# Optimization experiments

Hardware: AMD Instinct MI355X
Metric: run time of the kernel (lower is better)

Reference implementation:

```python
import jax, jax.numpy as jnp
import numpy as np

B, S, P, E, H, FF = 4, 16, 256, 768, 12, 3072
HD = E // H
LN_EPS = 1e-5


def _layernorm(x, g, b):
    m = jnp.mean(x, axis=-1, keepdims=True)
    v = jnp.mean((x - m) ** 2, axis=-1, keepdims=True)
    return (x - m) * jax.lax.rsqrt(v + LN_EPS) * g + b


def _qkv(x, wqkv, bqkv):
    # wqkv: [3, E, E] (in, out layout), bqkv: [3, E]
    qkv = jnp.einsum('bspe,tef->tbspf', x, wqkv) + bqkv[:, None, None, None, :]
    q, k, v = qkv
    b, s, p, e = x.shape
    shp = (b, s, p, H, HD)
    return q.reshape(shp), k.reshape(shp), v.reshape(shp)


def spatial_attn(x, wqkv, bqkv, wo, bo, g, beta):
    q, k, v = _qkv(x, wqkv, bqkv)  # [b,s,p,n,d]
    scale = 1.0 / np.sqrt(HD).astype(np.float32)
    scores = jnp.einsum('bsind,bsjnd->bsnij', q, k) * scale  # [b,s,n,p,p]
    attn = jax.nn.softmax(scores, axis=-1)
    out = jnp.einsum('bsnij,bsjnd->bsind', attn, v)  # [b,s,p,n,d]
    out = out.reshape(x.shape)
    out = out @ wo + bo
    return _layernorm(x + out, g, beta)


def temporal_attn(x, wqkv, bqkv, wo, bo, g, beta):
    q, k, v = _qkv(x, wqkv, bqkv)  # [b,s,p,n,d]
    scale = 1.0 / np.sqrt(HD).astype(np.float32)
    scores = jnp.einsum('bipnd,bjpnd->bpnij', q, k) * scale  # [b,p,n,s,s]
    s = x.shape[1]
    causal = jnp.tril(jnp.ones((s, s), dtype=bool))
    scores = jnp.where(causal, scores, jnp.float32(-jnp.inf))
    attn = jax.nn.softmax(scores, axis=-1)
    out = jnp.einsum('bpnij,bjpnd->bipnd', attn, v)  # [b,s,p,n,d]
    out = out.reshape(x.shape)
    out = out @ wo + bo
    return _layernorm(x + out, g, beta)


def ffn(x, w1, b1, w2, b2, g, beta):
    h = jax.nn.relu(x @ w1 + b1)
    out = h @ w2 + b2
    return _layernorm(x + out, g, beta)


def setup_inputs() -> dict:
    key = jax.random.key(0)
    ks = jax.random.split(key, 16)
    w = lambda k, shp: (jax.random.normal(k, shp, dtype=jnp.float32) * 0.02)
    inp = {
        'x': jax.random.normal(ks[0], (B, S, P, E), dtype=jnp.float32),
        'sa_wqkv': w(ks[1], (3, E, E)), 'sa_bqkv': jnp.zeros((3, E), jnp.float32),
        'sa_wo': w(ks[2], (E, E)), 'sa_bo': jnp.zeros((E,), jnp.float32),
        'sa_g': jnp.ones((E,), jnp.float32), 'sa_b': jnp.zeros((E,), jnp.float32),
        'ta_wqkv': w(ks[3], (3, E, E)), 'ta_bqkv': jnp.zeros((3, E), jnp.float32),
        'ta_wo': w(ks[4], (E, E)), 'ta_bo': jnp.zeros((E,), jnp.float32),
        'ta_g': jnp.ones((E,), jnp.float32), 'ta_b': jnp.zeros((E,), jnp.float32),
        'f_w1': w(ks[5], (E, FF)), 'f_b1': jnp.zeros((FF,), jnp.float32),
        'f_w2': w(ks[6], (FF, E)), 'f_b2': jnp.zeros((E,), jnp.float32),
        'f_g': jnp.ones((E,), jnp.float32), 'f_b': jnp.zeros((E,), jnp.float32),
    }
    return inp


def reference(x, sa_wqkv, sa_bqkv, sa_wo, sa_bo, sa_g, sa_b,
              ta_wqkv, ta_bqkv, ta_wo, ta_bo, ta_g, ta_b,
              f_w1, f_b1, f_w2, f_b2, f_g, f_b):
    x = spatial_attn(x, sa_wqkv, sa_bqkv, sa_wo, sa_bo, sa_g, sa_b)
    x = temporal_attn(x, ta_wqkv, ta_bqkv, ta_wo, ta_bo, ta_g, ta_b)
    x = ffn(x, f_w1, f_b1, f_w2, f_b2, f_g, f_b)
    return x
```

## Files before the change

### kernel.cpp

```cpp
#include <hip/hip_runtime.h>
#include <hip/hip_bf16.h>
#include <math.h>

constexpr int Bc = 4, Sc = 16, Pc = 256, Ec = 768, Hc = 12, HDc = 64, FFc = 3072;
constexpr int Mrows = Bc * Sc * Pc;
constexpr size_t ME = (size_t)Mrows * Ec;

typedef __attribute__((ext_vector_type(4))) float f32x4;
typedef __attribute__((ext_vector_type(8))) short s16x8;
typedef __attribute__((ext_vector_type(4))) short s16x4;

__device__ __forceinline__ short f2bf(float f) {
  union { float f; unsigned u; } v; v.f = f;
  unsigned r = (v.u + 0x7FFFu + ((v.u >> 16) & 1u)) >> 16;
  return (short)r;
}
__device__ __forceinline__ float bf2f(short s) {
  union { unsigned u; float f; } v; v.u = ((unsigned)(unsigned short)s) << 16;
  return v.f;
}

__device__ __forceinline__ void async16(const void* g, void* l) {
  __builtin_amdgcn_global_load_lds(
      (const __attribute__((address_space(1))) unsigned int*)g,
      (__attribute__((address_space(3))) unsigned int*)l, 16, 0, 0);
}

__global__ __launch_bounds__(256)
void f2bf_kernel(const float* __restrict__ in, short* __restrict__ out, int n8)
{
  int i = blockIdx.x * 256 + threadIdx.x;
  if (i >= n8) return;
  const float4* p = reinterpret_cast<const float4*>(in + (size_t)i * 8);
  float4 a = p[0], b = p[1];
  s16x8 o = { f2bf(a.x), f2bf(a.y), f2bf(a.z), f2bf(a.w),
              f2bf(b.x), f2bf(b.y), f2bf(b.z), f2bf(b.w) };
  *reinterpret_cast<s16x8*>(out + (size_t)i * 8) = o;
}

__global__ __launch_bounds__(256)
void wtrans_kernel(const float* __restrict__ Wg, short* __restrict__ Wtg,
                   int K, int N)
{
  const int z = blockIdx.z;
  const float* W  = Wg  + (size_t)z * K * N;
  short*       Wt = Wtg + (size_t)z * N * K;
  const int n0 = blockIdx.x * 64, k0 = blockIdx.y * 64;
  const int t = threadIdx.x;
  const int n  = n0 + (t >> 2);
  const int kc = k0 + (t & 3) * 16;
  short buf[16];
#pragma unroll
  for (int i = 0; i < 16; ++i)
    buf[i] = f2bf(W[(size_t)(kc + i) * N + n]);
  *reinterpret_cast<s16x8*>(&Wt[(size_t)n * K + kc])     = *reinterpret_cast<s16x8*>(&buf[0]);
  *reinterpret_cast<s16x8*>(&Wt[(size_t)n * K + kc + 8]) = *reinterpret_cast<s16x8*>(&buf[8]);
}

#define LDFRAG(base, row, kc) \
  (*reinterpret_cast<const s16x8*>((base) + (row) * 128 + ((((kc) ^ ((row) & 7)) << 4))))

#define PH_READS(Aslot, Bslot, q, LDB) \
  do { \
    if (LDB) { \
      _Pragma("unroll") \
      for (int nj = 0; nj < 4; ++nj) { \
        bfr[nj][0] = LDFRAG((Bslot), wc * 64 + nj * 16 + l16, g); \
        bfr[nj][1] = LDFRAG((Bslot), wc * 64 + nj * 16 + l16, 4 + g); \
      } \
    } \
    _Pragma("unroll") \
    for (int mi = 0; mi < 2; ++mi) { \
      afr[mi][0] = LDFRAG((Aslot), wr * 128 + ((q) * 2 + mi) * 16 + l16, g); \
      afr[mi][1] = LDFRAG((Aslot), wr * 128 + ((q) * 2 + mi) * 16 + l16, 4 + g); \
    } \
  } while (0)

#define PH_SYNC_MMA(q) \
  do { \
    __builtin_amdgcn_sched_barrier(0); \
    __builtin_amdgcn_s_barrier(); \
    asm volatile("s_waitcnt lgkmcnt(0)" ::: "memory"); \
    __builtin_amdgcn_sched_barrier(0); \
    __builtin_amdgcn_s_setprio(1); \
    _Pragma("unroll") \
    for (int mi = 0; mi < 2; ++mi) \
      _Pragma("unroll") \
      for (int nj = 0; nj < 4; ++nj) { \
        acc[(q) * 2 + mi][nj] = __builtin_amdgcn_mfma_f32_16x16x32_bf16( \
            afr[mi][0], bfr[nj][0], acc[(q) * 2 + mi][nj], 0, 0, 0); \
        acc[(q) * 2 + mi][nj] = __builtin_amdgcn_mfma_f32_16x16x32_bf16( \
            afr[mi][1], bfr[nj][1], acc[(q) * 2 + mi][nj], 0, 0, 0); \
      } \
    __builtin_amdgcn_s_setprio(0); \
  } while (0)

#define PH_END \
  do { __builtin_amdgcn_s_barrier(); __builtin_amdgcn_sched_barrier(0); } while (0)

#define PH_END_VM \
  do { \
    asm volatile("s_waitcnt vmcnt(4)" ::: "memory"); \
    __builtin_amdgcn_sched_barrier(0); \
    __builtin_amdgcn_s_barrier(); \
    __builtin_amdgcn_sched_barrier(0); \
  } while (0)

template<int OUT>
__global__ __launch_bounds__(512, 2)
void gemm256_kernel(const short* __restrict__ A, const short* __restrict__ Wt,
                    const float* __restrict__ biasg, const void* __restrict__ resv,
                    void* __restrict__ Cg, short* __restrict__ vt,
                    int M, int N, int K)
{
  __shared__ char smem[131072];
  const int z = blockIdx.z;
  const short* __restrict__ Wz = Wt + (size_t)z * (size_t)N * K;
  const float* __restrict__ bz = biasg + (size_t)z * N;

  const int nwg = gridDim.x;
  const int swz = ((int)blockIdx.x & 7) * (nwg >> 3) + ((int)blockIdx.x >> 3);
  const int NT = N >> 8;
  const int bm = (swz / NT) << 8;
  const int bn = (swz % NT) << 8;

  const int tid  = threadIdx.x;
  const int lane = tid & 63;
  const int wid  = tid >> 6;
  const int wr   = wid >> 2;
  const int wc   = wid & 3;
  const int l16  = lane & 15;
  const int g    = lane >> 4;

  char* const As0 = smem;
  char* const Bs0 = smem + 32768;
  char* const As1 = smem + 65536;
  char* const Bs1 = smem + 98304;

  const int srow = lane >> 3;
  const int scol = ((lane & 7) ^ srow) * 8;
  const int ldso = wid * 1024;

  auto stageG = [&](const short* __restrict__ G, int grow0, int k0, char* ldsHalf) {
    const size_t r0 = (size_t)(grow0 + wid * 8 + srow);
    async16(G + r0 * K + (k0 + scol), ldsHalf + ldso);
    async16(G + (r0 + 64) * K + (k0 + scol), ldsHalf + 8192 + ldso);
  };

  f32x4 acc[8][4];
  s16x8 bfr[4][2];
  s16x8 afr[2][2];
#pragma unroll
  for (int mi = 0; mi < 8; ++mi)
#pragma unroll
    for (int nj = 0; nj < 4; ++nj) acc[mi][nj] = f32x4{0.f, 0.f, 0.f, 0.f};

  const int ntile = K >> 6;
  const int nit   = ntile >> 1;

  stageG(A,  bm,        0,  As0);
  stageG(A,  bm + 128,  0,  As0 + 16384);
  stageG(Wz, bn,        0,  Bs0);
  stageG(Wz, bn + 128,  0,  Bs0 + 16384);
  stageG(Wz, bn,        64, Bs1);
  stageG(Wz, bn + 128,  64, Bs1 + 16384);
  asm volatile("s_waitcnt vmcnt(4)" ::: "memory");
  __builtin_amdgcn_sched_barrier(0);
  __builtin_amdgcn_s_barrier();

  for (int j = 0; j < nit; ++j) {
    const int t1k = (2 * j + 1) << 6;
    const int t2k = (2 * j + 2) << 6;
    const int t3k = (2 * j + 3) << 6;
    const bool s2 = (2 * j + 2) < ntile;
    const bool s3 = (2 * j + 3) < ntile;

    PH_READS(As0, Bs0, 0, true);
    stageG(A, bm, t1k, As1);
    PH_SYNC_MMA(0);
    PH_END;

    PH_READS(As0, Bs0, 1, false);
    stageG(A, bm + 128, t1k, As1 + 16384);
    PH_SYNC_MMA(1);
    PH_END;

    PH_READS(As0, Bs0, 2, false);
    if (s2) stageG(Wz, bn, t2k, Bs0);
    PH_SYNC_MMA(2);
    PH_END;

    PH_READS(As0, Bs0, 3, false);
    if (s2) stageG(Wz, bn + 128, t2k, Bs0 + 16384);
    PH_SYNC_MMA(3);
    PH_END_VM;

    PH_READS(As1, Bs1, 0, true);
    if (s2) stageG(A, bm, t2k, As0);
    PH_SYNC_MMA(0);
    PH_END;

    PH_READS(As1, Bs1, 1, false);
    if (s2) stageG(A, bm + 128, t2k, As0 + 16384);
    PH_SYNC_MMA(1);
    PH_END;

    PH_READS(As1, Bs1, 2, false);
    if (s3) stageG(Wz, bn, t3k, Bs1);
    PH_SYNC_MMA(2);
    PH_END;

    PH_READS(As1, Bs1, 3, false);
    if (s3) stageG(Wz, bn + 128, t3k, Bs1 + 16384);
    PH_SYNC_MMA(3);
    PH_END_VM;
  }

  const float* resf = (const float*)resv;
  const short* resb = (const short*)resv;
  short* Cb = (short*)Cg + (size_t)z * (size_t)M * N;
  float* Cf = (float*)Cg + (size_t)z * (size_t)M * N;

#pragma unroll
  for (int mi = 0; mi < 8; ++mi) {
    const int row0 = bm + wr * 128 + mi * 16 + g * 4;
#pragma unroll
    for (int nj = 0; nj < 4; ++nj) {
      const int col = bn + wc * 64 + nj * 16 + l16;
      if (OUT == 4 && z == 2) {
        const int bs2 = row0 >> 8, p0 = row0 & 255;
        const int h2 = col >> 6,  d2 = col & 63;
        const float bias = bz[col];
        s16x4 v = { f2bf(acc[mi][nj][0] + bias), f2bf(acc[mi][nj][1] + bias),
                    f2bf(acc[mi][nj][2] + bias), f2bf(acc[mi][nj][3] + bias) };
        *reinterpret_cast<s16x4*>(
            &vt[(((size_t)bs2 * 12 + h2) * 64 + d2) * 256 + p0]) = v;
      } else {
        const float bias = bz[col];
#pragma unroll
        for (int r = 0; r < 4; ++r) {
          float v = acc[mi][nj][r] + bias;
          size_t idx = (size_t)(row0 + r) * N + col;
          if (OUT == 2) v += resf[idx];
          if (OUT == 3) v += bf2f(resb[idx]);
          if (OUT == 1) v = fmaxf(v, 0.f);
          if (OUT == 2 || OUT == 3) Cf[idx] = v;
          else                      Cb[idx] = f2bf(v);
        }
      }
    }
  }
}

__global__ __launch_bounds__(256, 3)
void spatial_attn_kernel(const short* __restrict__ Qg, const short* __restrict__ Kg,
                         const short* __restrict__ Vt, short* __restrict__ Og)
{
  const int bs = blockIdx.x;
  const int h  = blockIdx.y;

  __shared__ short Pl[4 * 32 * 64];

  const int tid  = threadIdx.x;
  const int lane = tid & 63;
  const int wid  = tid >> 6;
  const int l16  = lane & 15;
  const int g    = lane >> 4;
  const int q0   = blockIdx.z * 128 + wid * 32;
  char* Pw = (char*)Pl + wid * 4096;

  const size_t rowbase = (size_t)(bs * 256) * 768 + h * 64;
  const size_t vbase   = ((size_t)bs * 12 + h) * 64 * 256;

  s16x8 qa[2][2];
#pragma unroll
  for (int m = 0; m < 2; ++m)
#pragma unroll
    for (int ks = 0; ks < 2; ++ks)
      qa[m][ks] = *reinterpret_cast<const s16x8*>(
          &Qg[rowbase + (size_t)(q0 + m * 16 + l16) * 768 + ks * 32 + g * 8]);

  float mrun[2][4], lrun[2][4];
  f32x4 oac[2][4];
#pragma unroll
  for (int m = 0; m < 2; ++m)
#pragma unroll
    for (int r = 0; r < 4; ++r) { mrun[m][r] = -INFINITY; lrun[m][r] = 0.f; }
#pragma unroll
  for (int m = 0; m < 2; ++m)
#pragma unroll
    for (int n = 0; n < 4; ++n) oac[m][n] = f32x4{0.f, 0.f, 0.f, 0.f};

#pragma unroll
  for (int t = 0; t < 4; ++t) {
    const int key0 = t * 64;
    f32x4 sc[2][4];
#pragma unroll
    for (int m = 0; m < 2; ++m)
#pragma unroll
      for (int n = 0; n < 4; ++n) sc[m][n] = f32x4{0.f, 0.f, 0.f, 0.f};
#pragma unroll
    for (int ks = 0; ks < 2; ++ks) {
      s16x8 kf[4];
#pragma unroll
      for (int n = 0; n < 4; ++n) {
        const int key = key0 + n * 16 + l16;
        kf[n] = *reinterpret_cast<const s16x8*>(
            &Kg[rowbase + (size_t)key * 768 + ks * 32 + g * 8]);
      }
#pragma unroll
      for (int m = 0; m < 2; ++m)
#pragma unroll
        for (int n = 0; n < 4; ++n)
          sc[m][n] = __builtin_amdgcn_mfma_f32_16x16x32_bf16(qa[m][ks], kf[n], sc[m][n], 0, 0, 0);
    }
#pragma unroll
    for (int m = 0; m < 2; ++m)
#pragma unroll
      for (int n = 0; n < 4; ++n)
#pragma unroll
        for (int r = 0; r < 4; ++r) sc[m][n][r] *= 0.125f;

#pragma unroll
    for (int m = 0; m < 2; ++m) {
#pragma unroll
      for (int r = 0; r < 4; ++r) {
        float mx = fmaxf(fmaxf(sc[m][0][r], sc[m][1][r]), fmaxf(sc[m][2][r], sc[m][3][r]));
#pragma unroll
        for (int mk = 1; mk < 16; mk <<= 1) mx = fmaxf(mx, __shfl_xor(mx, mk, 64));
        const float mnew = fmaxf(mrun[m][r], mx);
        const float corr = __expf(mrun[m][r] - mnew);
        mrun[m][r] = mnew;
        float rs = 0.f;
#pragma unroll
        for (int n = 0; n < 4; ++n) {
          float p = __expf(sc[m][n][r] - mnew);
          sc[m][n][r] = p;
          rs += p;
        }
#pragma unroll
        for (int mk = 1; mk < 16; mk <<= 1) rs += __shfl_xor(rs, mk, 64);
        lrun[m][r] = lrun[m][r] * corr + rs;
#pragma unroll
        for (int nd = 0; nd < 4; ++nd) oac[m][nd][r] *= corr;
      }
    }
#pragma unroll
    for (int m = 0; m < 2; ++m)
#pragma unroll
      for (int n = 0; n < 4; ++n)
#pragma unroll
        for (int r = 0; r < 4; ++r) {
          const int q = m * 16 + g * 4 + r;
          const int key = n * 16 + l16;
          const int byte = q * 128 + (((key >> 3) ^ (q & 7)) * 16) + (key & 7) * 2;
          *reinterpret_cast<short*>(Pw + byte) = f2bf(sc[m][n][r]);
        }
#pragma unroll
    for (int ks = 0; ks < 2; ++ks) {
      s16x8 pa[2], vf[4];
#pragma unroll
      for (int m = 0; m < 2; ++m) {
        const int q = m * 16 + l16;
        const int s = ks * 4 + g;
        pa[m] = *reinterpret_cast<const s16x8*>(Pw + q * 128 + ((s ^ (q & 7)) * 16));
      }
#pragma unroll
      for (int nd = 0; nd < 4; ++nd) {
        const int d = nd * 16 + l16;
        const int key = key0 + ks * 32 + g * 8;
        vf[nd] = *reinterpret_cast<const s16x8*>(&Vt[vbase + (size_t)d * 256 + key]);
      }
#pragma unroll
      for (int m = 0; m < 2; ++m)
#pragma unroll
        for (int nd = 0; nd < 4; ++nd)
          oac[m][nd] = __builtin_amdgcn_mfma_f32_16x16x32_bf16(pa[m], vf[nd], oac[m][nd], 0, 0, 0);
    }
  }

#pragma unroll
  for (int m = 0; m < 2; ++m)
#pragma unroll
    for (int r = 0; r < 4; ++r) {
      const float inv = 1.f / lrun[m][r];
#pragma unroll
      for (int nd = 0; nd < 4; ++nd) oac[m][nd][r] *= inv;
    }
#pragma unroll
  for (int m = 0; m < 2; ++m)
#pragma unroll
    for (int nd = 0; nd < 4; ++nd)
#pragma unroll
      for (int r = 0; r < 4; ++r) {
        const int q = m * 16 + g * 4 + r;
        const int d = nd * 16 + l16;
        const int byte = q * 128 + (((d >> 3) ^ (q & 7)) * 16) + (d & 7) * 2;
        *reinterpret_cast<short*>(Pw + byte) = f2bf(oac[m][nd][r]);
      }
#pragma unroll
  for (int it = 0; it < 4; ++it) {
    const int slot = it * 64 + lane;
    const int q = slot >> 3, sl = slot & 7;
    const int d0 = (sl ^ (q & 7)) * 8;
    s16x8 v = *reinterpret_cast<const s16x8*>(Pw + slot * 16);
    *reinterpret_cast<s16x8*>(
        &Og[rowbase + (size_t)(q0 + q) * 768 + d0]) = v;
  }
}

__global__ __launch_bounds__(192)
void temporal_attn_kernel(const short* __restrict__ Qg, const short* __restrict__ Kg,
                          const short* __restrict__ Vg, short* __restrict__ Og)
{
  const int bp = blockIdx.x;
  const int b = bp >> 8, p = bp & 255;
  const int tid = threadIdx.x;
  const int h = tid >> 4, i = tid & 15;

  const float scale = 0.125f;
  auto rowoff = [&](int s) {
    return ((size_t)(b * Sc + s) * Pc + p) * Ec + (size_t)h * HDc;
  };

  float q[HDc];
  {
    const short* qp = &Qg[rowoff(i)];
#pragma unroll
    for (int c = 0; c < 8; ++c) {
      s16x8 v = *reinterpret_cast<const s16x8*>(qp + c * 8);
#pragma unroll
      for (int e = 0; e < 8; ++e) q[c * 8 + e] = bf2f(v[e]) * scale;
    }
  }
  float m = -INFINITY, l = 0.f;
  float o[HDc];
#pragma unroll
  for (int d = 0; d < HDc; ++d) o[d] = 0.f;

  for (int j = 0; j <= i; ++j) {
    const short* kp = &Kg[rowoff(j)];
    float s = 0.f;
#pragma unroll
    for (int c = 0; c < 8; ++c) {
      s16x8 kv = *reinterpret_cast<const s16x8*>(kp + c * 8);
#pragma unroll
      for (int e = 0; e < 8; ++e) s += q[c * 8 + e] * bf2f(kv[e]);
    }
    float mn   = fmaxf(m, s);
    float corr = __expf(m - mn);
    float pw   = __expf(s - mn);
    l = l * corr + pw;
    const short* vp = &Vg[rowoff(j)];
#pragma unroll
    for (int c = 0; c < 8; ++c) {
      s16x8 vv = *reinterpret_cast<const s16x8*>(vp + c * 8);
#pragma unroll
      for (int e = 0; e < 8; ++e)
        o[c * 8 + e] = fmaf(pw, bf2f(vv[e]), o[c * 8 + e] * corr);
    }
    m = mn;
  }
  const float inv = 1.f / l;
  short* op = &Og[rowoff(i)];
#pragma unroll
  for (int c = 0; c < 8; ++c) {
    s16x8 v;
#pragma unroll
    for (int e = 0; e < 8; ++e) v[e] = f2bf(o[c * 8 + e] * inv);
    *reinterpret_cast<s16x8*>(op + c * 8) = v;
  }
}

template<bool OUTBF>
__global__ __launch_bounds__(256)
void layernorm_kernel(const float* __restrict__ U, const float* __restrict__ g,
                      const float* __restrict__ be, void* __restrict__ outv)
{
  const int tid  = threadIdx.x;
  const int lane = tid & 63, w = tid >> 6;
  const size_t row = (size_t)blockIdx.x * 4 + w;
  const float* u = U + row * Ec;

  float x[12];
#pragma unroll
  for (int c = 0; c < 3; ++c) {
    float4 v = *reinterpret_cast<const float4*>(&u[c * 256 + lane * 4]);
    x[c*4+0] = v.x; x[c*4+1] = v.y; x[c*4+2] = v.z; x[c*4+3] = v.w;
  }
  float s = 0.f;
#pragma unroll
  for (int k = 0; k < 12; ++k) s += x[k];
#pragma unroll
  for (int off = 32; off > 0; off >>= 1) s += __shfl_xor(s, off, 64);
  const float mean = s * (1.f / 768.f);

  float vs = 0.f;
#pragma unroll
  for (int k = 0; k < 12; ++k) { float d = x[k] - mean; vs += d * d; }
#pragma unroll
  for (int off = 32; off > 0; off >>= 1) vs += __shfl_xor(vs, off, 64);
  const float rs = rsqrtf(vs * (1.f / 768.f) + 1e-5f);

#pragma unroll
  for (int c = 0; c < 3; ++c) {
    int idx = c * 256 + lane * 4;
    float4 gv = *reinterpret_cast<const float4*>(&g[idx]);
    float4 bv = *reinterpret_cast<const float4*>(&be[idx]);
    float r0 = (x[c*4+0] - mean) * rs * gv.x + bv.x;
    float r1 = (x[c*4+1] - mean) * rs * gv.y + bv.y;
    float r2 = (x[c*4+2] - mean) * rs * gv.z + bv.z;
    float r3 = (x[c*4+3] - mean) * rs * gv.w + bv.w;
    if (OUTBF) {
      short* op = (short*)outv + row * Ec + idx;
      s16x4 v = { f2bf(r0), f2bf(r1), f2bf(r2), f2bf(r3) };
      *reinterpret_cast<s16x4*>(op) = v;
    } else {
      float* op = (float*)outv + row * Ec + idx;
      *reinterpret_cast<float4*>(op) = make_float4(r0, r1, r2, r3);
    }
  }
}

extern "C" void kernel_launch(void* const* d_in, const int* in_sizes, int n_in,
                              void* d_out, int out_size, void* d_ws, size_t ws_size,
                              hipStream_t stream)
{
  const float* x       = (const float*)d_in[0];
  const float* sa_wqkv = (const float*)d_in[1];
  const float* sa_bqkv = (const float*)d_in[2];
  const float* sa_wo   = (const float*)d_in[3];
  const float* sa_bo   = (const float*)d_in[4];
  const float* sa_g    = (const float*)d_in[5];
  const float* sa_b    = (const float*)d_in[6];
  const float* ta_wqkv = (const float*)d_in[7];
  const float* ta_bqkv = (const float*)d_in[8];
  const float* ta_wo   = (const float*)d_in[9];
  const float* ta_bo   = (const float*)d_in[10];
  const float* ta_g    = (const float*)d_in[11];
  const float* ta_b    = (const float*)d_in[12];
  const float* f_w1    = (const float*)d_in[13];
  const float* f_b1    = (const float*)d_in[14];
  const float* f_w2    = (const float*)d_in[15];
  const float* f_b2    = (const float*)d_in[16];
  const float* f_g     = (const float*)d_in[17];
  const float* f_b     = (const float*)d_in[18];

  float* out = (float*)d_out;

  constexpr size_t EE = (size_t)Ec * Ec;
  constexpr size_t WTOT = 3*EE + EE + 3*EE + EE + 2*(size_t)Ec*FFc;
  const size_t need = 14 * ME + 2 * WTOT;
  if (ws_size < need) return;

  short* Xb  = (short*)d_ws;
  short* Qb  = Xb + ME;
  short* Kb  = Qb + ME;
  short* Vtb = Qb + 2 * ME;
  short* Hb  = Qb;
  float* U   = (float*)(Xb + 5 * ME);
  short* Wtb = (short*)(U + ME);

  short* wt_sa_qkv = Wtb;
  short* wt_sa_wo  = wt_sa_qkv + 3 * EE;
  short* wt_ta_qkv = wt_sa_wo  + EE;
  short* wt_ta_wo  = wt_ta_qkv + 3 * EE;
  short* wt_f_w1   = wt_ta_wo  + EE;
  short* wt_f_w2   = wt_f_w1   + (size_t)Ec * FFc;

  wtrans_kernel<<<dim3(12, 12, 3), 256, 0, stream>>>(sa_wqkv, wt_sa_qkv, Ec, Ec);
  wtrans_kernel<<<dim3(12, 12, 1), 256, 0, stream>>>(sa_wo,   wt_sa_wo,  Ec, Ec);
  wtrans_kernel<<<dim3(12, 12, 3), 256, 0, stream>>>(ta_wqkv, wt_ta_qkv, Ec, Ec);
  wtrans_kernel<<<dim3(12, 12, 1), 256, 0, stream>>>(ta_wo,   wt_ta_wo,  Ec, Ec);
  wtrans_kernel<<<dim3(48, 12, 1), 256, 0, stream>>>(f_w1,    wt_f_w1,   Ec, FFc);
  wtrans_kernel<<<dim3(12, 48, 1), 256, 0, stream>>>(f_w2,    wt_f_w2,   FFc, Ec);
  f2bf_kernel<<<(int)(ME / 8 / 256), 256, 0, stream>>>(x, Xb, (int)(ME / 8));

  const int MT = Mrows / 256;
  const dim3 gQKV(MT * (Ec / 256), 1, 3);
  const dim3 gSQ (MT * (Ec / 256), 1, 1);
  const dim3 gFF1(MT * (FFc / 256), 1, 1);

  gemm256_kernel<4><<<gQKV, 512, 0, stream>>>(Xb, wt_sa_qkv, sa_bqkv, nullptr, Qb, Vtb, Mrows, Ec, Ec);
  spatial_attn_kernel<<<dim3(Bc * Sc, Hc, 2), 256, 0, stream>>>(Qb, Kb, Vtb, Qb);
  gemm256_kernel<2><<<gSQ, 512, 0, stream>>>(Qb, wt_sa_wo, sa_bo, x, U, nullptr, Mrows, Ec, Ec);
  layernorm_kernel<true><<<Mrows / 4, 256, 0, stream>>>(U, sa_g, sa_b, Xb);

  gemm256_kernel<0><<<gQKV, 512, 0, stream>>>(Xb, wt_ta_qkv, ta_bqkv, nullptr, Qb, nullptr, Mrows, Ec, Ec);
  temporal_attn_kernel<<<Bc * Pc, 192, 0, stream>>>(Qb, Kb, Vtb, Qb);
  gemm256_kernel<3><<<gSQ, 512, 0, stream>>>(Qb, wt_ta_wo, ta_bo, Xb, U, nullptr, Mrows, Ec, Ec);
  layernorm_kernel<true><<<Mrows / 4, 256, 0, stream>>>(U, ta_g, ta_b, Xb);

  gemm256_kernel<1><<<gFF1, 512, 0, stream>>>(Xb, wt_f_w1, f_b1, nullptr, Hb, nullptr, Mrows, FFc, Ec);
  gemm256_kernel<3><<<gSQ, 512, 0, stream>>>(Hb, wt_f_w2, f_b2, Xb, U, nullptr, Mrows, Ec, FFc);
  layernorm_kernel<false><<<Mrows / 4, 256, 0, stream>>>(U, f_g, f_b, out);
}
```

Baseline: 643.2 us.

## Use 128-row GEMM tiles for N=768 projections and stage temporal K/V in LDS

The GEMM kernel gains a BMT template parameter so the output projections and the FFN2 GEMM (N=768) run with 128x256 tiles. This doubles the grid for those launches, aiming to fill more CUs and reduce tail imbalance, at the cost of less reuse of the weight tile. The temporal attention kernel now cooperatively loads all 16 timesteps of K and V for one (b,p) into shared memory with a head-interleaved layout. The causal loop then reads LDS instead of repeatedly hitting global memory from each thread. Threads are remapped to head-fastest order (h = tid%12) for this.

Result: faster. 613.5 us (-4.6%).

```diff
diff --git a/kernel.cpp b/kernel.cpp
--- a/kernel.cpp
+++ b/kernel.cpp
@@ -70,9 +70,10 @@
       } \
     } \
     _Pragma("unroll") \
-    for (int mi = 0; mi < 2; ++mi) { \
-      afr[mi][0] = LDFRAG((Aslot), wr * 128 + ((q) * 2 + mi) * 16 + l16, g); \
-      afr[mi][1] = LDFRAG((Aslot), wr * 128 + ((q) * 2 + mi) * 16 + l16, 4 + g); \
+    for (int mi = 0; mi < BMT; ++mi) { \
+      const int arow = wr * (BMT * 64) + ((q) * BMT + mi) * 16 + l16; \
+      afr[mi][0] = LDFRAG((Aslot), arow, g); \
+      afr[mi][1] = LDFRAG((Aslot), arow, 4 + g); \
     } \
   } while (0)
 
@@ -84,13 +85,13 @@
     __builtin_amdgcn_sched_barrier(0); \
     __builtin_amdgcn_s_setprio(1); \
     _Pragma("unroll") \
-    for (int mi = 0; mi < 2; ++mi) \
+    for (int mi = 0; mi < BMT; ++mi) \
       _Pragma("unroll") \
       for (int nj = 0; nj < 4; ++nj) { \
-        acc[(q) * 2 + mi][nj] = __builtin_amdgcn_mfma_f32_16x16x32_bf16( \
-            afr[mi][0], bfr[nj][0], acc[(q) * 2 + mi][nj], 0, 0, 0); \
-        acc[(q) * 2 + mi][nj] = __builtin_amdgcn_mfma_f32_16x16x32_bf16( \
-            afr[mi][1], bfr[nj][1], acc[(q) * 2 + mi][nj], 0, 0, 0); \
+        acc[(q) * BMT + mi][nj] = __builtin_amdgcn_mfma_f32_16x16x32_bf16( \
+            afr[mi][0], bfr[nj][0], acc[(q) * BMT + mi][nj], 0, 0, 0); \
+        acc[(q) * BMT + mi][nj] = __builtin_amdgcn_mfma_f32_16x16x32_bf16( \
+            afr[mi][1], bfr[nj][1], acc[(q) * BMT + mi][nj], 0, 0, 0); \
       } \
     __builtin_amdgcn_s_setprio(0); \
   } while (0)
@@ -106,14 +107,15 @@
     __builtin_amdgcn_sched_barrier(0); \
   } while (0)
 
-template<int OUT>
+template<int OUT, int BMT>
 __global__ __launch_bounds__(512, 2)
 void gemm256_kernel(const short* __restrict__ A, const short* __restrict__ Wt,
                     const float* __restrict__ biasg, const void* __restrict__ resv,
                     void* __restrict__ Cg, short* __restrict__ vt,
                     int M, int N, int K)
 {
-  __shared__ char smem[131072];
+  constexpr int ASZ = BMT * 16384;
+  __shared__ char smem[2 * (ASZ + 32768)];
   const int z = blockIdx.z;
   const short* __restrict__ Wz = Wt + (size_t)z * (size_t)N * K;
   const float* __restrict__ bz = biasg + (size_t)z * N;
@@ -121,7 +123,7 @@
   const int nwg = gridDim.x;
   const int swz = ((int)blockIdx.x & 7) * (nwg >> 3) + ((int)blockIdx.x >> 3);
   const int NT = N >> 8;
-  const int bm = (swz / NT) << 8;
+  const int bm = (swz / NT) * (BMT * 128);
   const int bn = (swz % NT) << 8;
 
   const int tid  = threadIdx.x;
@@ -133,9 +135,9 @@
   const int g    = lane >> 4;
 
   char* const As0 = smem;
-  char* const Bs0 = smem + 32768;
-  char* const As1 = smem + 65536;
-  char* const Bs1 = smem + 98304;
+  char* const Bs0 = smem + ASZ;
+  char* const As1 = smem + ASZ + 32768;
+  char* const Bs1 = smem + 2 * ASZ + 32768;
 
   const int srow = lane >> 3;
   const int scol = ((lane & 7) ^ srow) * 8;
@@ -147,23 +149,23 @@
     async16(G + (r0 + 64) * K + (k0 + scol), ldsHalf + 8192 + ldso);
   };
 
-  f32x4 acc[8][4];
+  f32x4 acc[BMT * 4][4];
   s16x8 bfr[4][2];
-  s16x8 afr[2][2];
-#pragma unroll
-  for (int mi = 0; mi < 8; ++mi)
+  s16x8 afr[BMT][2];
+#pragma unroll
+  for (int mi = 0; mi < BMT * 4; ++mi)
 #pragma unroll
     for (int nj = 0; nj < 4; ++nj) acc[mi][nj] = f32x4{0.f, 0.f, 0.f, 0.f};
 
   const int ntile = K >> 6;
   const int nit   = ntile >> 1;
 
-  stageG(A,  bm,        0,  As0);
-  stageG(A,  bm + 128,  0,  As0 + 16384);
-  stageG(Wz, bn,        0,  Bs0);
-  stageG(Wz, bn + 128,  0,  Bs0 + 16384);
-  stageG(Wz, bn,        64, Bs1);
-  stageG(Wz, bn + 128,  64, Bs1 + 16384);
+  stageG(A, bm, 0, As0);
+  if (BMT == 2) stageG(A, bm + 128, 0, As0 + 16384);
+  stageG(Wz, bn,       0,  Bs0);
+  stageG(Wz, bn + 128, 0,  Bs0 + 16384);
+  stageG(Wz, bn,       64, Bs1);
+  stageG(Wz, bn + 128, 64, Bs1 + 16384);
   asm volatile("s_waitcnt vmcnt(4)" ::: "memory");
   __builtin_amdgcn_sched_barrier(0);
   __builtin_amdgcn_s_barrier();
@@ -181,7 +183,7 @@
     PH_END;
 
     PH_READS(As0, Bs0, 1, false);
-    stageG(A, bm + 128, t1k, As1 + 16384);
+    if (BMT == 2) stageG(A, bm + 128, t1k, As1 + 16384);
     PH_SYNC_MMA(1);
     PH_END;
 
@@ -201,7 +203,7 @@
     PH_END;
 
     PH_READS(As1, Bs1, 1, false);
-    if (s2) stageG(A, bm + 128, t2k, As0 + 16384);
+    if (BMT == 2) { if (s2) stageG(A, bm + 128, t2k, As0 + 16384); }
     PH_SYNC_MMA(1);
     PH_END;
 
@@ -222,8 +224,8 @@
   float* Cf = (float*)Cg + (size_t)z * (size_t)M * N;
 
 #pragma unroll
-  for (int mi = 0; mi < 8; ++mi) {
-    const int row0 = bm + wr * 128 + mi * 16 + g * 4;
+  for (int mi = 0; mi < BMT * 4; ++mi) {
+    const int row0 = bm + wr * (BMT * 64) + mi * 16 + g * 4;
 #pragma unroll
     for (int nj = 0; nj < 4; ++nj) {
       const int col = bn + wc * 64 + nj * 16 + l16;
@@ -415,35 +417,54 @@
 {
   const int bp = blockIdx.x;
   const int b = bp >> 8, p = bp & 255;
+
+  __shared__ short Ks[16 * 768];
+  __shared__ short Vs[16 * 768];
+
   const int tid = threadIdx.x;
-  const int h = tid >> 4, i = tid & 15;
-
+  const size_t gbase = ((size_t)(b * 16) * 256 + p) * 768;
+  constexpr int SROW = 256 * 768;
+
+  {
+    const int half = tid / 96;
+    const int cc   = tid - half * 96;
+    const int c    = cc & 7, hs = cc >> 3;
+    const int ldso = (c * 12 + hs) * 8;
+#pragma unroll
+    for (int it = 0; it < 8; ++it) {
+      const int s = it * 2 + half;
+      const size_t ga = gbase + (size_t)s * SROW + cc * 8;
+      *reinterpret_cast<s16x8*>(&Ks[s * 768 + ldso]) =
+          *reinterpret_cast<const s16x8*>(&Kg[ga]);
+      *reinterpret_cast<s16x8*>(&Vs[s * 768 + ldso]) =
+          *reinterpret_cast<const s16x8*>(&Vg[ga]);
+    }
+  }
+  __syncthreads();
+
+  const int h = tid % 12, i = tid / 12;
   const float scale = 0.125f;
-  auto rowoff = [&](int s) {
-    return ((size_t)(b * Sc + s) * Pc + p) * Ec + (size_t)h * HDc;
-  };
+  const size_t qoff = gbase + (size_t)i * SROW + h * 64;
 
   float q[HDc];
-  {
-    const short* qp = &Qg[rowoff(i)];
-#pragma unroll
-    for (int c = 0; c < 8; ++c) {
-      s16x8 v = *reinterpret_cast<const s16x8*>(qp + c * 8);
-#pragma unroll
-      for (int e = 0; e < 8; ++e) q[c * 8 + e] = bf2f(v[e]) * scale;
-    }
-  }
+#pragma unroll
+  for (int c = 0; c < 8; ++c) {
+    s16x8 v = *reinterpret_cast<const s16x8*>(&Qg[qoff + c * 8]);
+#pragma unroll
+    for (int e = 0; e < 8; ++e) q[c * 8 + e] = bf2f(v[e]) * scale;
+  }
+
   float m = -INFINITY, l = 0.f;
   float o[HDc];
 #pragma unroll
   for (int d = 0; d < HDc; ++d) o[d] = 0.f;
 
   for (int j = 0; j <= i; ++j) {
-    const short* kp = &Kg[rowoff(j)];
+    const short* kr = &Ks[j * 768];
     float s = 0.f;
 #pragma unroll
     for (int c = 0; c < 8; ++c) {
-      s16x8 kv = *reinterpret_cast<const s16x8*>(kp + c * 8);
+      s16x8 kv = *reinterpret_cast<const s16x8*>(kr + (c * 12 + h) * 8);
 #pragma unroll
       for (int e = 0; e < 8; ++e) s += q[c * 8 + e] * bf2f(kv[e]);
     }
@@ -451,10 +472,10 @@
     float corr = __expf(m - mn);
     float pw   = __expf(s - mn);
     l = l * corr + pw;
-    const short* vp = &Vg[rowoff(j)];
+    const short* vr = &Vs[j * 768];
 #pragma unroll
     for (int c = 0; c < 8; ++c) {
-      s16x8 vv = *reinterpret_cast<const s16x8*>(vp + c * 8);
+      s16x8 vv = *reinterpret_cast<const s16x8*>(vr + (c * 12 + h) * 8);
 #pragma unroll
       for (int e = 0; e < 8; ++e)
         o[c * 8 + e] = fmaf(pw, bf2f(vv[e]), o[c * 8 + e] * corr);
@@ -462,7 +483,7 @@
     m = mn;
   }
   const float inv = 1.f / l;
-  short* op = &Og[rowoff(i)];
+  short* op = &Og[qoff];
 #pragma unroll
   for (int c = 0; c < 8; ++c) {
     s16x8 v;
@@ -576,22 +597,21 @@
   wtrans_kernel<<<dim3(12, 48, 1), 256, 0, stream>>>(f_w2,    wt_f_w2,   FFc, Ec);
   f2bf_kernel<<<(int)(ME / 8 / 256), 256, 0, stream>>>(x, Xb, (int)(ME / 8));
 
-  const int MT = Mrows / 256;
-  const dim3 gQKV(MT * (Ec / 256), 1, 3);
-  const dim3 gSQ (MT * (Ec / 256), 1, 1);
-  const dim3 gFF1(MT * (FFc / 256), 1, 1);
-
-  gemm256_kernel<4><<<gQKV, 512, 0, stream>>>(Xb, wt_sa_qkv, sa_bqkv, nullptr, Qb, Vtb, Mrows, Ec, Ec);
+  const dim3 gQKV((Mrows / 256) * (Ec / 256), 1, 3);
+  const dim3 gSQ ((Mrows / 128) * (Ec / 256), 1, 1);
+  const dim3 gFF1((Mrows / 256) * (FFc / 256), 1, 1);
+
+  gemm256_kernel<4, 2><<<gQKV, 512, 0, stream>>>(Xb, wt_sa_qkv, sa_bqkv, nullptr, Qb, Vtb, Mrows, Ec, Ec);
   spatial_attn_kernel<<<dim3(Bc * Sc, Hc, 2), 256, 0, stream>>>(Qb, Kb, Vtb, Qb);
-  gemm256_kernel<2><<<gSQ, 512, 0, stream>>>(Qb, wt_sa_wo, sa_bo, x, U, nullptr, Mrows, Ec, Ec);
+  gemm256_kernel<2, 1><<<gSQ, 512, 0, stream>>>(Qb, wt_sa_wo, sa_bo, x, U, nullptr, Mrows, Ec, Ec);
   layernorm_kernel<true><<<Mrows / 4, 256, 0, stream>>>(U, sa_g, sa_b, Xb);
 
-  gemm256_kernel<0><<<gQKV, 512, 0, stream>>>(Xb, wt_ta_qkv, ta_bqkv, nullptr, Qb, nullptr, Mrows, Ec, Ec);
+  gemm256_kernel<0, 2><<<gQKV, 512, 0, stream>>>(Xb, wt_ta_qkv, ta_bqkv, nullptr, Qb, nullptr, Mrows, Ec, Ec);
   temporal_attn_kernel<<<Bc * Pc, 192, 0, stream>>>(Qb, Kb, Vtb, Qb);
-  gemm256_kernel<3><<<gSQ, 512, 0, stream>>>(Qb, wt_ta_wo, ta_bo, Xb, U, nullptr, Mrows, Ec, Ec);
+  gemm256_kernel<3, 1><<<gSQ, 512, 0, stream>>>(Qb, wt_ta_wo, ta_bo, Xb, U, nullptr, Mrows, Ec, Ec);
   layernorm_kernel<true><<<Mrows / 4, 256, 0, stream>>>(U, ta_g, ta_b, Xb);
 
-  gemm256_kernel<1><<<gFF1, 512, 0, stream>>>(Xb, wt_f_w1, f_b1, nullptr, Hb, nullptr, Mrows, FFc, Ec);
-  gemm256_kernel<3><<<gSQ, 512, 0, stream>>>(Hb, wt_f_w2, f_b2, Xb, U, nullptr, Mrows, Ec, FFc);
+  gemm256_kernel<1, 2><<<gFF1, 512, 0, stream>>>(Xb, wt_f_w1, f_b1, nullptr, Hb, nullptr, Mrows, FFc, Ec);
+  gemm256_kernel<3, 1><<<gSQ, 512, 0, stream>>>(Hb, wt_f_w2, f_b2, Xb, U, nullptr, Mrows, Ec, FFc);
   layernorm_kernel<false><<<Mrows / 4, 256, 0, stream>>>(U, f_g, f_b, out);
 }
```
